# Kernel optimization log

Measured on AMD Instinct MI355X. Metric: run time of the kernel, lower is better.

## Reference

```python
import jax, jax.numpy as jnp
import numpy as np

NUM_HEAD = 16

def setup_inputs() -> dict:
    rk = jax.random.key(0)
    k1, k2, k3, k4, k5 = jax.random.split(rk, 5)
    B, Sq, Skv, D = 4, 2048, 2048, 1024
    return {
        "query": jax.random.normal(k1, (B, Sq, D), dtype=jnp.float32),
        "key":   jax.random.normal(k2, (B, Skv, D), dtype=jnp.float32),
        "value": jax.random.normal(k3, (B, Skv, D), dtype=jnp.float32),
        "W": jax.random.normal(k4, (D, D), dtype=jnp.float32) * (D ** -0.5),
        "b": jax.random.normal(k5, (D,), dtype=jnp.float32) * 0.01,
    }

def reference(query, key, value, W, b):
    B, Sq, D = query.shape
    H = NUM_HEAD
    hd = D // H
    # chunk(num_head, -1) == split last dim into H contiguous heads
    q = query.reshape(B, Sq, H, hd)
    k = key.reshape(B, -1, H, hd)
    v = value.reshape(B, -1, H, hd)
    # scores[b,h,q,k] = (Q_h K_h^T) / sqrt(embedding_dim)  (full dim, per source)
    scores = jnp.einsum('bqhd,bkhd->bhqk', q, k) / jnp.sqrt(jnp.float32(D))
    # nn.Softmax(dim=1) on a [B, q, kv] matrix -> softmax over the QUERY axis
    attn = jax.nn.softmax(scores, axis=2)
    out = jnp.einsum('bhqk,bkhd->bqhd', attn, v).reshape(B, Sq, D)
    # final linear: x @ W^T + b
    return out @ W.T + b
```

## Files before the change

### kernel.cpp

```cpp
#include <hip/hip_runtime.h>

#define NH    16
#define HD    64
#define SQ    2048
#define SKV   2048
#define DM    1024

typedef __attribute__((ext_vector_type(8))) __bf16 bf16x8;
typedef __attribute__((ext_vector_type(4))) __bf16 bf16x4;
typedef __attribute__((ext_vector_type(4))) float  f32x4;

#define ASYNC16(gp, lp)                                                        \
    __builtin_amdgcn_global_load_lds(                                          \
        (const __attribute__((address_space(1))) void*)(gp),                   \
        (__attribute__((address_space(3))) void*)(lp), 16, 0, 0)

#if __has_builtin(__builtin_amdgcn_exp2f)
#define EXPS(x) __builtin_amdgcn_exp2f((x) * 0.04508422f)
#else
#define EXPS(x) __expf((x) * 0.03125f)
#endif

static __device__ __forceinline__ int swz(int row, int chunk) {
    return (row << 6) + (((chunk) ^ (row & 7)) << 3);
}

static __device__ __forceinline__ bf16x4 cvt4(float4 v) {
    bf16x4 r;
    r[0] = (__bf16)v.x; r[1] = (__bf16)v.y; r[2] = (__bf16)v.z; r[3] = (__bf16)v.w;
    return r;
}

__global__ void kprep_all(const float* __restrict__ q, const float* __restrict__ k,
                          const float* __restrict__ W,
                          __bf16* __restrict__ Qh, __bf16* __restrict__ Kh,
                          __bf16* __restrict__ Wb) {
    int bid = blockIdx.x;
    if (bid < 8192) {
        const float* src = (bid < 4096) ? q : k;
        __bf16* dst = (bid < 4096) ? Qh : Kh;
        size_t g = (size_t)(bid & 4095) * 256 + threadIdx.x;
        size_t o = g * 8;
        int c  = (int)(o & 63);
        int s  = (int)((o >> 6) & 2047);
        int bh = (int)(o >> 17);
        int b = bh >> 4, h = bh & 15;
        const float* p = src + ((size_t)(b * SQ + s)) * DM + h * HD + c;
        float4 v0 = *(const float4*)p;
        float4 v1 = *(const float4*)(p + 4);
        bf16x8 r;
        r[0] = (__bf16)v0.x; r[1] = (__bf16)v0.y; r[2] = (__bf16)v0.z; r[3] = (__bf16)v0.w;
        r[4] = (__bf16)v1.x; r[5] = (__bf16)v1.y; r[6] = (__bf16)v1.z; r[7] = (__bf16)v1.w;
        *(bf16x8*)(dst + o) = r;
    } else {
        int i = (bid - 8192) * 256 + threadIdx.x;
        float4 v = *(const float4*)(W + (size_t)i * 4);
        *(bf16x4*)(Wb + (size_t)i * 4) = cvt4(v);
    }
}

__global__ __launch_bounds__(256, 2) void kz(const __bf16* __restrict__ Qh,
                                             const __bf16* __restrict__ Kh,
                                             const float* __restrict__ v,
                                             __bf16* __restrict__ Vt) {
    const int bh = blockIdx.x;
    const int kb = blockIdx.y;
    const int b = bh >> 4, h = bh & 15;
    const int t = threadIdx.x;
    const int w = t >> 6, lane = t & 63;
    const int lo16 = lane & 15, quad = lane >> 4;
    const int wub = (t & 192) << 3;

    __shared__ __bf16 Ks[256 * 64];
    __shared__ __bf16 Qs[2][64 * 64];
    __shared__ float  Zs[256];

    const __bf16* kbase = Kh + ((size_t)bh * SKV + kb * 256) * HD;
    const __bf16* qbase = Qh + (size_t)bh * SQ * HD;

#pragma unroll
    for (int i = 0; i < 8; ++i) {
        int ci = i * 256 + t;
        int row = ci >> 3;
        int c = (ci & 7) ^ (row & 7);
        ASYNC16(kbase + row * 64 + c * 8, &Ks[i * 2048 + wub]);
    }
#pragma unroll
    for (int i = 0; i < 2; ++i) {
        int ci = i * 256 + t;
        int row = ci >> 3;
        int c = (ci & 7) ^ (row & 7);
        ASYNC16(qbase + row * 64 + c * 8, &Qs[0][i * 2048 + wub]);
    }
    __syncthreads();

    bf16x8 bk[4][2];
#pragma unroll
    for (int nt = 0; nt < 4; ++nt)
#pragma unroll
        for (int dh = 0; dh < 2; ++dh)
            bk[nt][dh] = *(const bf16x8*)(&Ks[swz(w * 64 + nt * 16 + lo16, dh * 4 + quad)]);

    float zacc[4] = {0.f, 0.f, 0.f, 0.f};

    for (int qt = 0; qt < 32; ++qt) {
        const int cur = qt & 1, nxt = cur ^ 1;
        if (qt < 31) {
#pragma unroll
            for (int i = 0; i < 2; ++i) {
                int ci = i * 256 + t;
                int row = ci >> 3;
                int c = (ci & 7) ^ (row & 7);
                ASYNC16(qbase + (size_t)(qt + 1) * 64 * HD + row * 64 + c * 8,
                        &Qs[nxt][i * 2048 + wub]);
            }
        }

#pragma unroll
        for (int mt = 0; mt < 4; ++mt) {
            bf16x8 aq0 = *(const bf16x8*)(&Qs[cur][swz(mt * 16 + lo16, quad)]);
            bf16x8 aq1 = *(const bf16x8*)(&Qs[cur][swz(mt * 16 + lo16, 4 + quad)]);
#pragma unroll
            for (int nt = 0; nt < 4; ++nt) {
                f32x4 acc = {0.f, 0.f, 0.f, 0.f};
                acc = __builtin_amdgcn_mfma_f32_16x16x32_bf16(aq0, bk[nt][0], acc, 0, 0, 0);
                acc = __builtin_amdgcn_mfma_f32_16x16x32_bf16(aq1, bk[nt][1], acc, 0, 0, 0);
                zacc[nt] += EXPS(acc[0]) + EXPS(acc[1]) + EXPS(acc[2]) + EXPS(acc[3]);
            }
        }
        __syncthreads();
    }

#pragma unroll
    for (int nt = 0; nt < 4; ++nt) {
        float s = zacc[nt];
        s += __shfl_xor(s, 16, 64);
        s += __shfl_xor(s, 32, 64);
        if (lane < 16) Zs[w * 64 + nt * 16 + lane] = s;
    }
    __syncthreads();

    {
        float rz = 1.0f / Zs[t];
        const float* vrow = v + ((size_t)(b * SKV) + kb * 256 + t) * DM + h * HD;
        size_t vtb = (size_t)bh * HD * SKV + kb * 256 + t;
#pragma unroll
        for (int dc = 0; dc < 4; ++dc) {
            float4 a0 = *(const float4*)(vrow + dc * 16 + 0);
            float4 a1 = *(const float4*)(vrow + dc * 16 + 4);
            float4 a2 = *(const float4*)(vrow + dc * 16 + 8);
            float4 a3 = *(const float4*)(vrow + dc * 16 + 12);
            float tmp[16] = {a0.x, a0.y, a0.z, a0.w, a1.x, a1.y, a1.z, a1.w,
                             a2.x, a2.y, a2.z, a2.w, a3.x, a3.y, a3.z, a3.w};
#pragma unroll
            for (int j = 0; j < 16; ++j)
                Vt[vtb + (size_t)(dc * 16 + j) * SKV] = (__bf16)(tmp[j] * rz);
        }
    }
}

__global__ __launch_bounds__(256, 2) void kattn(const __bf16* __restrict__ Qh,
                                                const __bf16* __restrict__ Kh,
                                                const __bf16* __restrict__ Vt,
                                                __bf16* __restrict__ O) {
    const int bh = blockIdx.x;
    const int qb = blockIdx.y;
    const int b = bh >> 4, h = bh & 15;
    const int t = threadIdx.x;
    const int w = t >> 6, lane = t & 63;
    const int lo16 = lane & 15, quad = lane >> 4;
    const int wub = (t & 192) << 3;

    __shared__ __bf16 Ks[2][64 * 64];
    __shared__ __bf16 Vts[2][64 * 64];
    __shared__ __bf16 QE[256 * 64];

    const __bf16* qgbase = Qh + ((size_t)bh * SQ + qb * 256) * HD;
    const __bf16* kgbase = Kh + (size_t)bh * SKV * HD;
    const __bf16* vtgbase = Vt + (size_t)bh * HD * SKV;

#pragma unroll
    for (int i = 0; i < 8; ++i) {
        int ci = i * 256 + t;
        int row = ci >> 3;
        int c = (ci & 7) ^ (row & 7);
        ASYNC16(qgbase + row * 64 + c * 8, &QE[i * 2048 + wub]);
    }
#pragma unroll
    for (int i = 0; i < 2; ++i) {
        int ci = i * 256 + t;
        int row = ci >> 3;
        int c = (ci & 7) ^ (row & 7);
        ASYNC16(kgbase + row * 64 + c * 8, &Ks[0][i * 2048 + wub]);
        ASYNC16(vtgbase + (size_t)row * SKV + c * 8, &Vts[0][i * 2048 + wub]);
    }
    __syncthreads();

    bf16x8 qf[4][2];
#pragma unroll
    for (int qt = 0; qt < 4; ++qt)
#pragma unroll
        for (int dh = 0; dh < 2; ++dh)
            qf[qt][dh] = *(const bf16x8*)(&QE[swz(w * 64 + qt * 16 + lo16, dh * 4 + quad)]);

    f32x4 oacc[4][4];
    f32x4 zero = {0.f, 0.f, 0.f, 0.f};
#pragma unroll
    for (int qt = 0; qt < 4; ++qt)
#pragma unroll
        for (int nt = 0; nt < 4; ++nt)
            oacc[qt][nt] = zero;

    __bf16* Ew = &QE[w * 64 * 64];

    for (int kt = 0; kt < 32; ++kt) {
        const int cur = kt & 1, nxt = cur ^ 1;
        if (kt < 31) {
#pragma unroll
            for (int i = 0; i < 2; ++i) {
                int ci = i * 256 + t;
                int row = ci >> 3;
                int c = (ci & 7) ^ (row & 7);
                ASYNC16(kgbase + (size_t)(kt + 1) * 64 * HD + row * 64 + c * 8,
                        &Ks[nxt][i * 2048 + wub]);
                ASYNC16(vtgbase + (size_t)row * SKV + (kt + 1) * 64 + c * 8,
                        &Vts[nxt][i * 2048 + wub]);
            }
        }

#pragma unroll
        for (int ktile = 0; ktile < 4; ++ktile) {
            bf16x8 ak0 = *(const bf16x8*)(&Ks[cur][swz(ktile * 16 + lo16, quad)]);
            bf16x8 ak1 = *(const bf16x8*)(&Ks[cur][swz(ktile * 16 + lo16, 4 + quad)]);
#pragma unroll
            for (int qt = 0; qt < 4; ++qt) {
                f32x4 s = zero;
                s = __builtin_amdgcn_mfma_f32_16x16x32_bf16(ak0, qf[qt][0], s, 0, 0, 0);
                s = __builtin_amdgcn_mfma_f32_16x16x32_bf16(ak1, qf[qt][1], s, 0, 0, 0);
                bf16x4 e;
                e[0] = (__bf16)EXPS(s[0]);
                e[1] = (__bf16)EXPS(s[1]);
                e[2] = (__bf16)EXPS(s[2]);
                e[3] = (__bf16)EXPS(s[3]);
                int er = qt * 16 + lo16;
                *(bf16x4*)(&Ew[(er << 6) + ((((2 * ktile + (quad >> 1))) ^ (er & 7)) << 3)
                               + (quad & 1) * 4]) = e;
            }
        }

#pragma unroll
        for (int kk2 = 0; kk2 < 2; ++kk2) {
            bf16x8 ae[4];
#pragma unroll
            for (int qt = 0; qt < 4; ++qt)
                ae[qt] = *(const bf16x8*)(&Ew[swz(qt * 16 + lo16, kk2 * 4 + quad)]);
#pragma unroll
            for (int nt = 0; nt < 4; ++nt) {
                bf16x8 bv = *(const bf16x8*)(&Vts[cur][swz(nt * 16 + lo16, kk2 * 4 + quad)]);
#pragma unroll
                for (int qt = 0; qt < 4; ++qt)
                    oacc[qt][nt] = __builtin_amdgcn_mfma_f32_16x16x32_bf16(ae[qt], bv, oacc[qt][nt], 0, 0, 0);
            }
        }
        __syncthreads();
    }

    size_t obase = ((size_t)(b * SQ) + qb * 256 + w * 64) * DM + h * HD;
#pragma unroll
    for (int qt = 0; qt < 4; ++qt)
#pragma unroll
        for (int nt = 0; nt < 4; ++nt)
#pragma unroll
            for (int r = 0; r < 4; ++r)
                O[obase + (size_t)(qt * 16 + quad * 4 + r) * DM + nt * 16 + lo16] =
                    (__bf16)oacc[qt][nt][r];
}

__global__ __launch_bounds__(256, 2) void kproj(const __bf16* __restrict__ A,
                                                const __bf16* __restrict__ Wb,
                                                const float* __restrict__ bias,
                                                float* __restrict__ out) {
    const int nb = blockIdx.x;
    const int mb = blockIdx.y;
    const int t = threadIdx.x;
    const int w = t >> 6, lane = t & 63;
    const int lo16 = lane & 15, quad = lane >> 4;
    const int wm = w & 1, wn = w >> 1;
    const int wub = (t & 192) << 3;

    __shared__ __bf16 As[2][128 * 64];
    __shared__ __bf16 Bs[2][128 * 64];

    f32x4 acc[4][4];
    f32x4 zero = {0.f, 0.f, 0.f, 0.f};
#pragma unroll
    for (int mt = 0; mt < 4; ++mt)
#pragma unroll
        for (int nt = 0; nt < 4; ++nt)
            acc[mt][nt] = zero;

    const __bf16* abase = A + (size_t)(mb * 128) * DM;
    const __bf16* wbase = Wb + (size_t)(nb * 128) * DM;

#pragma unroll
    for (int i = 0; i < 4; ++i) {
        int ci = i * 256 + t;
        int row = ci >> 3;
        int c = (ci & 7) ^ (row & 7);
        ASYNC16(abase + (size_t)row * DM + c * 8, &As[0][i * 2048 + wub]);
        ASYNC16(wbase + (size_t)row * DM + c * 8, &Bs[0][i * 2048 + wub]);
    }
    __syncthreads();

    for (int kt = 0; kt < 16; ++kt) {
        const int cur = kt & 1, nxt = cur ^ 1;
        if (kt < 15) {
#pragma unroll
            for (int i = 0; i < 4; ++i) {
                int ci = i * 256 + t;
                int row = ci >> 3;
                int c = (ci & 7) ^ (row & 7);
                ASYNC16(abase + (size_t)row * DM + (kt + 1) * 64 + c * 8, &As[nxt][i * 2048 + wub]);
                ASYNC16(wbase + (size_t)row * DM + (kt + 1) * 64 + c * 8, &Bs[nxt][i * 2048 + wub]);
            }
        }

#pragma unroll
        for (int ks = 0; ks < 2; ++ks) {
            bf16x8 av[4], bv[4];
#pragma unroll
            for (int mt = 0; mt < 4; ++mt)
                av[mt] = *(const bf16x8*)(&As[cur][swz(wm * 64 + mt * 16 + lo16, ks * 4 + quad)]);
#pragma unroll
            for (int nt = 0; nt < 4; ++nt)
                bv[nt] = *(const bf16x8*)(&Bs[cur][swz(wn * 64 + nt * 16 + lo16, ks * 4 + quad)]);
#pragma unroll
            for (int mt = 0; mt < 4; ++mt)
#pragma unroll
                for (int nt = 0; nt < 4; ++nt)
                    acc[mt][nt] = __builtin_amdgcn_mfma_f32_16x16x32_bf16(av[mt], bv[nt], acc[mt][nt], 0, 0, 0);
        }
        __syncthreads();
    }

    const int col0 = nb * 128 + wn * 64;
    const int row0 = mb * 128 + wm * 64;
#pragma unroll
    for (int nt = 0; nt < 4; ++nt) {
        float bb = bias[col0 + nt * 16 + lo16];
#pragma unroll
        for (int mt = 0; mt < 4; ++mt)
#pragma unroll
            for (int r = 0; r < 4; ++r)
                out[(size_t)(row0 + mt * 16 + quad * 4 + r) * DM + col0 + nt * 16 + lo16] =
                    acc[mt][nt][r] + bb;
    }
}

extern "C" void kernel_launch(void* const* d_in, const int* in_sizes, int n_in,
                              void* d_out, int out_size, void* d_ws, size_t ws_size,
                              hipStream_t stream) {
    const float* q    = (const float*)d_in[0];
    const float* k    = (const float*)d_in[1];
    const float* v    = (const float*)d_in[2];
    const float* W    = (const float*)d_in[3];
    const float* bias = (const float*)d_in[4];
    float* out = (float*)d_out;

    char* ws = (char*)d_ws;
    __bf16* Qh = (__bf16*)ws;
    __bf16* Kh = (__bf16*)(ws + (16u << 20));
    __bf16* Vt = (__bf16*)(ws + (32u << 20));
    __bf16* Wb = (__bf16*)(ws + (48u << 20));
    __bf16* O  = (__bf16*)(ws + (50u << 20));

    kprep_all<<<dim3(9216), 256, 0, stream>>>(q, k, W, Qh, Kh, Wb);
    kz       <<<dim3(64, 8), 256, 0, stream>>>(Qh, Kh, v, Vt);
    kattn    <<<dim3(64, 8), 256, 0, stream>>>(Qh, Kh, Vt, O);
    kproj    <<<dim3(8, 64), 256, 0, stream>>>(O, Wb, bias, out);
}
```

Measured before the change: 294.4 us.

## Keep exp tiles in registers via 16x16x16 MFMA; halve kz tile for occupancy

Result: no change. 298.3 us (+1.3%).

```diff
diff --git a/kernel.cpp b/kernel.cpp
--- a/kernel.cpp
+++ b/kernel.cpp
@@ -9,6 +9,7 @@
 typedef __attribute__((ext_vector_type(8))) __bf16 bf16x8;
 typedef __attribute__((ext_vector_type(4))) __bf16 bf16x4;
 typedef __attribute__((ext_vector_type(4))) float  f32x4;
+typedef __attribute__((ext_vector_type(4))) short  s16x4;
 
 #define ASYNC16(gp, lp)                                                        \
     __builtin_amdgcn_global_load_lds(                                          \
@@ -19,6 +20,19 @@
 #define EXPS(x) __builtin_amdgcn_exp2f((x) * 0.04508422f)
 #else
 #define EXPS(x) __expf((x) * 0.03125f)
+#endif
+
+#if __has_builtin(__builtin_amdgcn_mfma_f32_16x16x16bf16_1k)
+static __device__ __forceinline__ f32x4 mfma16(bf16x4 a, bf16x4 b, f32x4 c) {
+    return __builtin_amdgcn_mfma_f32_16x16x16bf16_1k(
+        __builtin_bit_cast(s16x4, a), __builtin_bit_cast(s16x4, b), c, 0, 0, 0);
+}
+#else
+static __device__ __forceinline__ f32x4 mfma16(bf16x4 a, bf16x4 b, f32x4 c) {
+    asm volatile("s_nop 1\n\tv_mfma_f32_16x16x16_bf16 %0, %1, %2, %0"
+                 : "+v"(c) : "v"(a), "v"(b));
+    return c;
+}
 #endif
 
 static __device__ __forceinline__ int swz(int row, int chunk) {
@@ -59,7 +73,7 @@
     }
 }
 
-__global__ __launch_bounds__(256, 2) void kz(const __bf16* __restrict__ Qh,
+__global__ __launch_bounds__(256, 4) void kz(const __bf16* __restrict__ Qh,
                                              const __bf16* __restrict__ Kh,
                                              const float* __restrict__ v,
                                              __bf16* __restrict__ Vt) {
@@ -71,15 +85,15 @@
     const int lo16 = lane & 15, quad = lane >> 4;
     const int wub = (t & 192) << 3;
 
-    __shared__ __bf16 Ks[256 * 64];
+    __shared__ __bf16 Ks[128 * 64];
     __shared__ __bf16 Qs[2][64 * 64];
-    __shared__ float  Zs[256];
-
-    const __bf16* kbase = Kh + ((size_t)bh * SKV + kb * 256) * HD;
+    __shared__ float  Zs[128];
+
+    const __bf16* kbase = Kh + ((size_t)bh * SKV + kb * 128) * HD;
     const __bf16* qbase = Qh + (size_t)bh * SQ * HD;
 
 #pragma unroll
-    for (int i = 0; i < 8; ++i) {
+    for (int i = 0; i < 4; ++i) {
         int ci = i * 256 + t;
         int row = ci >> 3;
         int c = (ci & 7) ^ (row & 7);
@@ -94,14 +108,14 @@
     }
     __syncthreads();
 
-    bf16x8 bk[4][2];
-#pragma unroll
-    for (int nt = 0; nt < 4; ++nt)
+    bf16x8 bk[2][2];
+#pragma unroll
+    for (int nt = 0; nt < 2; ++nt)
 #pragma unroll
         for (int dh = 0; dh < 2; ++dh)
-            bk[nt][dh] = *(const bf16x8*)(&Ks[swz(w * 64 + nt * 16 + lo16, dh * 4 + quad)]);
-
-    float zacc[4] = {0.f, 0.f, 0.f, 0.f};
+            bk[nt][dh] = *(const bf16x8*)(&Ks[swz(w * 32 + nt * 16 + lo16, dh * 4 + quad)]);
+
+    float zacc[2] = {0.f, 0.f};
 
     for (int qt = 0; qt < 32; ++qt) {
         const int cur = qt & 1, nxt = cur ^ 1;
@@ -121,7 +135,7 @@
             bf16x8 aq0 = *(const bf16x8*)(&Qs[cur][swz(mt * 16 + lo16, quad)]);
             bf16x8 aq1 = *(const bf16x8*)(&Qs[cur][swz(mt * 16 + lo16, 4 + quad)]);
 #pragma unroll
-            for (int nt = 0; nt < 4; ++nt) {
+            for (int nt = 0; nt < 2; ++nt) {
                 f32x4 acc = {0.f, 0.f, 0.f, 0.f};
                 acc = __builtin_amdgcn_mfma_f32_16x16x32_bf16(aq0, bk[nt][0], acc, 0, 0, 0);
                 acc = __builtin_amdgcn_mfma_f32_16x16x32_bf16(aq1, bk[nt][1], acc, 0, 0, 0);
@@ -132,20 +146,22 @@
     }
 
 #pragma unroll
-    for (int nt = 0; nt < 4; ++nt) {
+    for (int nt = 0; nt < 2; ++nt) {
         float s = zacc[nt];
         s += __shfl_xor(s, 16, 64);
         s += __shfl_xor(s, 32, 64);
-        if (lane < 16) Zs[w * 64 + nt * 16 + lane] = s;
+        if (lane < 16) Zs[w * 32 + nt * 16 + lane] = s;
     }
     __syncthreads();
 
     {
-        float rz = 1.0f / Zs[t];
-        const float* vrow = v + ((size_t)(b * SKV) + kb * 256 + t) * DM + h * HD;
-        size_t vtb = (size_t)bh * HD * SKV + kb * 256 + t;
-#pragma unroll
-        for (int dc = 0; dc < 4; ++dc) {
+        int kk = t & 127, dh2 = t >> 7;
+        float rz = 1.0f / Zs[kk];
+        int kfull = kb * 128 + kk;
+        const float* vrow = v + ((size_t)(b * SKV) + kfull) * DM + h * HD + dh2 * 32;
+        size_t vtb = (size_t)bh * HD * SKV + (size_t)(dh2 * 32) * SKV + kfull;
+#pragma unroll
+        for (int dc = 0; dc < 2; ++dc) {
             float4 a0 = *(const float4*)(vrow + dc * 16 + 0);
             float4 a1 = *(const float4*)(vrow + dc * 16 + 4);
             float4 a2 = *(const float4*)(vrow + dc * 16 + 8);
@@ -173,7 +189,7 @@
 
     __shared__ __bf16 Ks[2][64 * 64];
     __shared__ __bf16 Vts[2][64 * 64];
-    __shared__ __bf16 QE[256 * 64];
+    __shared__ __bf16 Qstage[256 * 64];
 
     const __bf16* qgbase = Qh + ((size_t)bh * SQ + qb * 256) * HD;
     const __bf16* kgbase = Kh + (size_t)bh * SKV * HD;
@@ -184,7 +200,7 @@
         int ci = i * 256 + t;
         int row = ci >> 3;
         int c = (ci & 7) ^ (row & 7);
-        ASYNC16(qgbase + row * 64 + c * 8, &QE[i * 2048 + wub]);
+        ASYNC16(qgbase + row * 64 + c * 8, &Qstage[i * 2048 + wub]);
     }
 #pragma unroll
     for (int i = 0; i < 2; ++i) {
@@ -201,7 +217,7 @@
     for (int qt = 0; qt < 4; ++qt)
 #pragma unroll
         for (int dh = 0; dh < 2; ++dh)
-            qf[qt][dh] = *(const bf16x8*)(&QE[swz(w * 64 + qt * 16 + lo16, dh * 4 + quad)]);
+            qf[qt][dh] = *(const bf16x8*)(&Qstage[swz(w * 64 + qt * 16 + lo16, dh * 4 + quad)]);
 
     f32x4 oacc[4][4];
     f32x4 zero = {0.f, 0.f, 0.f, 0.f};
@@ -210,8 +226,6 @@
 #pragma unroll
         for (int nt = 0; nt < 4; ++nt)
             oacc[qt][nt] = zero;
-
-    __bf16* Ew = &QE[w * 64 * 64];
 
     for (int kt = 0; kt < 32; ++kt) {
         const int cur = kt & 1, nxt = cur ^ 1;
@@ -228,10 +242,11 @@
             }
         }
 
-#pragma unroll
-        for (int ktile = 0; ktile < 4; ++ktile) {
-            bf16x8 ak0 = *(const bf16x8*)(&Ks[cur][swz(ktile * 16 + lo16, quad)]);
-            bf16x8 ak1 = *(const bf16x8*)(&Ks[cur][swz(ktile * 16 + lo16, 4 + quad)]);
+        bf16x4 ef[4][4];
+#pragma unroll
+        for (int kg = 0; kg < 4; ++kg) {
+            bf16x8 ak0 = *(const bf16x8*)(&Ks[cur][swz(kg * 16 + lo16, quad)]);
+            bf16x8 ak1 = *(const bf16x8*)(&Ks[cur][swz(kg * 16 + lo16, 4 + quad)]);
 #pragma unroll
             for (int qt = 0; qt < 4; ++qt) {
                 f32x4 s = zero;
@@ -242,28 +257,27 @@
                 e[1] = (__bf16)EXPS(s[1]);
                 e[2] = (__bf16)EXPS(s[2]);
                 e[3] = (__bf16)EXPS(s[3]);
-                int er = qt * 16 + lo16;
-                *(bf16x4*)(&Ew[(er << 6) + ((((2 * ktile + (quad >> 1))) ^ (er & 7)) << 3)
-                               + (quad & 1) * 4]) = e;
-            }
-        }
-
-#pragma unroll
-        for (int kk2 = 0; kk2 < 2; ++kk2) {
-            bf16x8 ae[4];
-#pragma unroll
-            for (int qt = 0; qt < 4; ++qt)
-                ae[qt] = *(const bf16x8*)(&Ew[swz(qt * 16 + lo16, kk2 * 4 + quad)]);
-#pragma unroll
-            for (int nt = 0; nt < 4; ++nt) {
-                bf16x8 bv = *(const bf16x8*)(&Vts[cur][swz(nt * 16 + lo16, kk2 * 4 + quad)]);
+                ef[qt][kg] = e;
+            }
+        }
+
+#pragma unroll
+        for (int nt = 0; nt < 4; ++nt) {
+#pragma unroll
+            for (int kg = 0; kg < 4; ++kg) {
+                int row = nt * 16 + lo16;
+                int chunk = kg * 2 + (quad >> 1);
+                bf16x4 bv = *(const bf16x4*)(
+                    &Vts[cur][(row << 6) + ((chunk ^ (row & 7)) << 3) + ((quad & 1) << 2)]);
 #pragma unroll
                 for (int qt = 0; qt < 4; ++qt)
-                    oacc[qt][nt] = __builtin_amdgcn_mfma_f32_16x16x32_bf16(ae[qt], bv, oacc[qt][nt], 0, 0, 0);
+                    oacc[qt][nt] = mfma16(ef[qt][kg], bv, oacc[qt][nt]);
             }
         }
         __syncthreads();
     }
+
+    asm volatile("s_nop 7\n\ts_nop 7" ::: );
 
     size_t obase = ((size_t)(b * SQ) + qb * 256 + w * 64) * DM + h * HD;
 #pragma unroll
@@ -375,7 +389,7 @@
     __bf16* O  = (__bf16*)(ws + (50u << 20));
 
     kprep_all<<<dim3(9216), 256, 0, stream>>>(q, k, W, Qh, Kh, Wb);
-    kz       <<<dim3(64, 8), 256, 0, stream>>>(Qh, Kh, v, Vt);
+    kz       <<<dim3(64, 16), 256, 0, stream>>>(Qh, Kh, v, Vt);
     kattn    <<<dim3(64, 8), 256, 0, stream>>>(Qh, Kh, Vt, O);
     kproj    <<<dim3(8, 64), 256, 0, stream>>>(O, Wb, bias, out);
 }
```
